# Performance work log

Hardware: AMD Instinct MI355X
Metric: run time of the kernel (lower is better)

The kernel has to match this reference:

```python
import jax, jax.numpy as jnp
import numpy as np

N, E, F_IN, F_OUT, K = 10000, 640000, 256, 64, 4


def setup_inputs() -> dict:
    key = jax.random.key(0)
    ks = jax.random.split(key, 8)
    feat = jax.random.normal(ks[0], (N, F_IN), dtype=jnp.float32)
    feat_a = jax.random.normal(ks[1], (N, F_IN), dtype=jnp.float32)
    edge_index = jax.random.randint(ks[2], (2, E), 0, N)
    graph_neigh = jax.random.uniform(ks[3], (N, N), dtype=jnp.float32)
    W = jax.random.normal(ks[4], ((K + 1) * F_IN, F_OUT), dtype=jnp.float32) * 0.05
    Wb = jax.random.normal(ks[5], (F_OUT, F_OUT), dtype=jnp.float32) * 0.05
    b = jnp.zeros((), dtype=jnp.float32)
    return {"feat": feat, "feat_a": feat_a, "edge_index": edge_index,
            "graph_neigh": graph_neigh, "W": W, "Wb": Wb, "b": b}


def _sym_norm(edge_index, num_nodes):
    # add_remaining_self_loops with all-ones weights: drop existing self-loops,
    # append a weight-1 self loop per node (fill_value=1, improved=False)
    row, col = edge_index[0], edge_index[1]
    w = jnp.where(row == col, 0.0, 1.0).astype(jnp.float32)
    loop = jnp.arange(num_nodes)
    row = jnp.concatenate([row, loop])
    col = jnp.concatenate([col, loop])
    w = jnp.concatenate([w, jnp.ones((num_nodes,), jnp.float32)])
    deg = jax.ops.segment_sum(w, row, num_segments=num_nodes)
    dis = jnp.where(deg > 0, jax.lax.rsqrt(deg), 0.0)  # inf -> 0
    norm = dis[row] * w * dis[col]
    return row, col, norm


def _comb_unweighted(x, row, col, norm, k_hops):
    # K-hop propagation: out[dst] += norm * x[src]; concat hops 0..K
    xs = [x]
    for _ in range(k_hops):
        msg = norm[:, None] * xs[-1][row]          # gather + scale  [E', F]
        xs.append(jax.ops.segment_sum(msg, col, num_segments=x.shape[0]))
    return jnp.concatenate(xs, axis=1)             # [N, F*(K+1)]


def _avg_readout(emb, mask):
    vsum = mask @ emb                              # [N, F_OUT]
    row_sum = jnp.sum(mask, axis=1, keepdims=True)
    g = vsum / row_sum
    nrm = jnp.linalg.norm(g, axis=1, keepdims=True)
    return g / jnp.maximum(nrm, 1e-12)             # F.normalize p=2


def _disc(c, h_pl, h_mi, Wb, b):
    # nn.Bilinear(n_h, n_h, 1): sc = h^T Wb c + b, per node
    sc1 = jnp.einsum('nd,de,ne->n', h_pl, Wb, c) + b
    sc2 = jnp.einsum('nd,de,ne->n', h_mi, Wb, c) + b
    return jnp.stack([sc1, sc2], axis=1)           # [N, 2]


def reference(feat, feat_a, edge_index, graph_neigh, W, Wb, b):
    row, col, norm = _sym_norm(edge_index, feat.shape[0])
    h = _comb_unweighted(feat, row, col, norm, K) @ W
    h_a = _comb_unweighted(feat_a, row, col, norm, K) @ W
    emb = jax.nn.relu(h)
    emb_a = jax.nn.relu(h_a)
    g = jax.nn.sigmoid(_avg_readout(emb, graph_neigh))
    g_a = jax.nn.sigmoid(_avg_readout(emb_a, graph_neigh))
    ret = _disc(g, emb, emb_a, Wb, b)
    ret_a = _disc(g_a, emb_a, emb, Wb, b)
    return emb, ret, ret_a
```

## Files before the change

kernel.cpp:

```cpp
#include <hip/hip_runtime.h>
#include <hip/hip_bf16.h>
#include <hip/hip_fp16.h>

typedef float f32x4 __attribute__((ext_vector_type(4)));
typedef short s16x8 __attribute__((ext_vector_type(8)));
typedef unsigned int u32x4 __attribute__((ext_vector_type(4)));

#define F_IN 256
#define F_OUT 64
#define KSPLIT 9
#define HBLK 120

static __device__ __forceinline__ short f2bf(float f){
  union { float f; unsigned u; } x; x.f = f;
  unsigned r = (x.u + 0x7FFFu + ((x.u >> 16) & 1u)) >> 16;
  return (short)r;
}

static __device__ __forceinline__ unsigned pack_rtne(float f0, float f1){
  return ((unsigned)(unsigned short)f2bf(f0)) | ((unsigned)(unsigned short)f2bf(f1) << 16);
}

static __device__ __forceinline__ unsigned pack_trunc(float f0, float f1){
  return (__float_as_uint(f0) >> 16) | (__float_as_uint(f1) & 0xFFFF0000u);
}

static __device__ __forceinline__ float bf_lo(unsigned u){ return __uint_as_float(u << 16); }
static __device__ __forceinline__ float bf_hi(unsigned u){ return __uint_as_float(u & 0xFFFF0000u); }
static __device__ __forceinline__ float h16(unsigned u){
  return __half2float(__ushort_as_half((unsigned short)(u >> 16)));
}

union FragU { u32x4 u; s16x8 s; };


__global__ void wt_kernel(const float* __restrict__ W, short* __restrict__ WT){
  int idx = blockIdx.x * blockDim.x + threadIdx.x;
  if (idx < 5 * 64 * 256){
    int k = idx & 255, c = (idx >> 8) & 63, by = idx >> 14;
    WT[idx] = f2bf(W[(size_t)(by * 256 + k) * 64 + c]);
  }
}


__global__ __launch_bounds__(1024) void hist_kernel(const int* __restrict__ ei, int E,
                                                    unsigned* __restrict__ blkcntP, int n){
  __shared__ unsigned bins[10240];
  int tid = threadIdx.x;
  int per = (E + HBLK - 1) / HBLK;
  int e0 = blockIdx.x * per, e1 = min(E, e0 + per);

  for (int i = tid; i < n; i += 1024) bins[i] = 0u;
  __syncthreads();
  for (int e = e0 + tid; e < e1; e += 1024){
    int r = ei[e], c = ei[E + e];
    if (r != c){
      atomicAdd(&bins[c], 1u);
      atomicAdd(&bins[r], 0x10000u);
    }
  }
  __syncthreads();
  for (int i = tid; i < n; i += 1024)
    blkcntP[(size_t)blockIdx.x * n + i] = bins[i];
}


__global__ void sumcnt_kernel(const unsigned* __restrict__ blkcntP,
                              int* __restrict__ counts, int* __restrict__ deg, int n){
  int bin = blockIdx.x * blockDim.x + threadIdx.x;
  if (bin >= n) return;
  int cc = 0, rc = 0;
  #pragma unroll 8
  for (int blk = 0; blk < HBLK; ++blk){
    unsigned v = blkcntP[(size_t)blk * n + bin];
    cc += (int)(v & 0xFFFFu);
    rc += (int)(v >> 16);
  }
  counts[bin] = cc;
  deg[bin] = rc;
}


__global__ __launch_bounds__(1024) void scan_kernel(const int* __restrict__ counts,
                                                    const int* __restrict__ deg,
                                                    float* __restrict__ dis,
                                                    float* __restrict__ selfnorm,
                                                    int* __restrict__ offsets, int n){
  const int C = 10;
  __shared__ int vals[10240];
  __shared__ int wsums[16];
  int tid = threadIdx.x, wid = tid >> 6, lane = tid & 63;
  for (int i = tid; i < 10240; i += 1024) vals[i] = (i < n) ? counts[i] : 0;
  for (int i = tid; i < n; i += 1024){
    float d = (float)(deg[i] + 1);
    dis[i] = rsqrtf(d);
    selfnorm[i] = 1.0f / d;
  }
  __syncthreads();
  int base = tid * C;
  int s = 0;
  #pragma unroll
  for (int i = 0; i < C; ++i) s += vals[base + i];
  int x = s;
  #pragma unroll
  for (int off = 1; off < 64; off <<= 1){
    int y = __shfl_up(x, off);
    if (lane >= off) x += y;
  }
  if (lane == 63) wsums[wid] = x;
  __syncthreads();
  if (wid == 0){
    int v = (lane < 16) ? wsums[lane] : 0;
    int xx = v;
    #pragma unroll
    for (int off = 1; off < 16; off <<= 1){
      int y = __shfl_up(xx, off);
      if (lane >= off) xx += y;
    }
    if (lane < 16) wsums[lane] = xx - v;
  }
  __syncthreads();
  int run = (x - s) + wsums[wid];
  if (tid == 1023) offsets[n] = run + s;
  #pragma unroll
  for (int i = 0; i < C; ++i){ int v = vals[base + i]; vals[base + i] = run; run += v; }
  __syncthreads();
  for (int i = tid; i < 10240; i += 1024)
    if (i < n) offsets[i] = vals[i];
}


__global__ void blkbase_kernel(const int* __restrict__ offsets, const unsigned* __restrict__ blkcntP,
                               int* __restrict__ blkbase, int n){
  int bin = blockIdx.x * blockDim.x + threadIdx.x;
  if (bin >= n) return;
  int run = offsets[bin];
  #pragma unroll 8
  for (int blk = 0; blk < HBLK; ++blk){
    blkbase[(size_t)blk * n + bin] = run;
    run += (int)(blkcntP[(size_t)blk * n + bin] & 0xFFFFu);
  }
}


__global__ __launch_bounds__(1024) void fill_kernel(const int* __restrict__ ei, int E,
                                                    const float* __restrict__ dis,
                                                    const int* __restrict__ blkbase,
                                                    unsigned* __restrict__ csr, int n){
  __shared__ int bins[10240];
  int tid = threadIdx.x;
  int per = (E + HBLK - 1) / HBLK;
  int e0 = blockIdx.x * per, e1 = min(E, e0 + per);
  for (int i = tid; i < n; i += 1024) bins[i] = blkbase[(size_t)blockIdx.x * n + i];
  __syncthreads();
  for (int e = e0 + tid; e < e1; e += 1024){
    int r = ei[e], c = ei[E + e];
    if (r == c) continue;
    int pos = atomicAdd(&bins[c], 1);
    unsigned h = (unsigned)__half_as_ushort(__float2half(dis[r] * dis[c]));
    csr[pos] = (unsigned)r | (h << 16);
  }
}


__global__ __launch_bounds__(320) void fgemm_kernel(const float* __restrict__ X0,
                                                    const float* __restrict__ X1,
                                                    const short* __restrict__ WT,
                                                    float* __restrict__ Yc0,
                                                    unsigned* __restrict__ YcB,
                                                    short* __restrict__ t0bf, int M){
  __shared__ float Xs[16][260];
  int tid = threadIdx.x;
  int w = tid >> 6, l = tid & 63, lr = l & 15, g = l >> 4;
  int row0 = blockIdx.x * 16, bz = blockIdx.y;
  const float* X = bz ? X1 : X0;
  for (int i = tid; i < 1024; i += 320){
    int r = i >> 6, c4 = (i & 63) << 2;
    *(f32x4*)&Xs[r][c4] = *(const f32x4*)(X + (size_t)(row0 + r) * F_IN + c4);
  }
  __syncthreads();

  s16x8 afr[8];
  #pragma unroll
  for (int it = 0; it < 8; ++it){
    f32x4 x0 = *(const f32x4*)&Xs[lr][it * 32 + g * 8];
    f32x4 x1 = *(const f32x4*)&Xs[lr][it * 32 + g * 8 + 4];
    FragU af;
    af.u[0] = pack_rtne(x0[0], x0[1]); af.u[1] = pack_rtne(x0[2], x0[3]);
    af.u[2] = pack_rtne(x1[0], x1[1]); af.u[3] = pack_rtne(x1[2], x1[3]);
    afr[it] = af.s;
  }

  int by = w;
  f32x4 acc[4];
  #pragma unroll
  for (int ct = 0; ct < 4; ++ct) acc[ct] = (f32x4){0,0,0,0};
  const s16x8* bp[4];
  #pragma unroll
  for (int ct = 0; ct < 4; ++ct)
    bp[ct] = (const s16x8*)(WT + ((size_t)by * 64 + ct * 16 + lr) * F_IN + g * 8);
  #pragma unroll
  for (int it = 0; it < 8; ++it)
    #pragma unroll
    for (int ct = 0; ct < 4; ++ct)
      acc[ct] = __builtin_amdgcn_mfma_f32_16x16x32_bf16(afr[it], bp[ct][it * 4], acc[ct], 0, 0, 0);

  if (by == 0){
    float* yp = Yc0 + (size_t)bz * 64;
    #pragma unroll
    for (int ct = 0; ct < 4; ++ct)
      #pragma unroll
      for (int i = 0; i < 4; ++i)
        yp[(size_t)(row0 + g * 4 + i) * 128 + ct * 16 + lr] = acc[ct][i];
  } else if (by <= 3){
    unsigned* yb = YcB + (size_t)(by - 1) * (M >> 1) * 128 + (size_t)bz * 64;
    #pragma unroll
    for (int ct = 0; ct < 4; ++ct)
      #pragma unroll
      for (int i = 0; i < 4; i += 2){
        int grow = row0 + g * 4 + i;
        yb[(size_t)(grow >> 1) * 128 + ct * 16 + lr] = pack_rtne(acc[ct][i], acc[ct][i + 1]);
      }
  } else {
    short* tb = t0bf + (size_t)bz * 64;
    #pragma unroll
    for (int ct = 0; ct < 4; ++ct)
      #pragma unroll
      for (int i = 0; i < 4; ++i)
        tb[(size_t)(row0 + g * 4 + i) * 128 + ct * 16 + lr] = f2bf(acc[ct][i]);
  }
}


__global__ __launch_bounds__(256) void gather_kernel(const void* __restrict__ Yk,
    const unsigned* __restrict__ tinb, const int* __restrict__ offsets,
    const unsigned* __restrict__ csr, const float* __restrict__ selfnorm,
    unsigned* __restrict__ toutb, float* __restrict__ toutf, int n, int wantf, int ykbf){
  int wid = threadIdx.x >> 6, lane = threadIdx.x & 63;
  int node = blockIdx.x * 4 + wid;
  if (node >= n) return;
  int e0 = offsets[node], e1 = offsets[node + 1];
  float sn = selfnorm[node];
  unsigned t0 = tinb[(size_t)node * 64 + lane];
  float ykx, yky;
  if (ykbf){
    const unsigned* yp = (const unsigned*)Yk + (size_t)(node >> 1) * 128 + lane * 2;
    unsigned u0 = yp[0], u1 = yp[1];
    if (node & 1){ ykx = bf_hi(u0); yky = bf_hi(u1); }
    else         { ykx = bf_lo(u0); yky = bf_lo(u1); }
  } else {
    float2 yk = ((const float2*)Yk)[(size_t)node * 64 + lane];
    ykx = yk.x; yky = yk.y;
  }
  float ax = ykx + sn * bf_lo(t0);
  float ay = yky + sn * bf_hi(t0);
  int i = e0;
  for (; i + 8 <= e1; i += 8){
    unsigned q0 = csr[i],   q1 = csr[i+1], q2 = csr[i+2], q3 = csr[i+3];
    unsigned q4 = csr[i+4], q5 = csr[i+5], q6 = csr[i+6], q7 = csr[i+7];
    unsigned v0 = tinb[(size_t)(q0 & 0xFFFFu) * 64 + lane];
    unsigned v1 = tinb[(size_t)(q1 & 0xFFFFu) * 64 + lane];
    unsigned v2 = tinb[(size_t)(q2 & 0xFFFFu) * 64 + lane];
    unsigned v3 = tinb[(size_t)(q3 & 0xFFFFu) * 64 + lane];
    unsigned v4 = tinb[(size_t)(q4 & 0xFFFFu) * 64 + lane];
    unsigned v5 = tinb[(size_t)(q5 & 0xFFFFu) * 64 + lane];
    unsigned v6 = tinb[(size_t)(q6 & 0xFFFFu) * 64 + lane];
    unsigned v7 = tinb[(size_t)(q7 & 0xFFFFu) * 64 + lane];
    float w0 = h16(q0), w1 = h16(q1), w2 = h16(q2), w3 = h16(q3);
    float w4 = h16(q4), w5 = h16(q5), w6 = h16(q6), w7 = h16(q7);
    ax += w0 * bf_lo(v0); ay += w0 * bf_hi(v0);
    ax += w1 * bf_lo(v1); ay += w1 * bf_hi(v1);
    ax += w2 * bf_lo(v2); ay += w2 * bf_hi(v2);
    ax += w3 * bf_lo(v3); ay += w3 * bf_hi(v3);
    ax += w4 * bf_lo(v4); ay += w4 * bf_hi(v4);
    ax += w5 * bf_lo(v5); ay += w5 * bf_hi(v5);
    ax += w6 * bf_lo(v6); ay += w6 * bf_hi(v6);
    ax += w7 * bf_lo(v7); ay += w7 * bf_hi(v7);
  }
  for (; i + 4 <= e1; i += 4){
    unsigned q0 = csr[i], q1 = csr[i+1], q2 = csr[i+2], q3 = csr[i+3];
    unsigned v0 = tinb[(size_t)(q0 & 0xFFFFu) * 64 + lane];
    unsigned v1 = tinb[(size_t)(q1 & 0xFFFFu) * 64 + lane];
    unsigned v2 = tinb[(size_t)(q2 & 0xFFFFu) * 64 + lane];
    unsigned v3 = tinb[(size_t)(q3 & 0xFFFFu) * 64 + lane];
    float w0 = h16(q0), w1 = h16(q1), w2 = h16(q2), w3 = h16(q3);
    ax += w0 * bf_lo(v0); ay += w0 * bf_hi(v0);
    ax += w1 * bf_lo(v1); ay += w1 * bf_hi(v1);
    ax += w2 * bf_lo(v2); ay += w2 * bf_hi(v2);
    ax += w3 * bf_lo(v3); ay += w3 * bf_hi(v3);
  }
  for (; i < e1; ++i){
    unsigned q = csr[i];
    float w = h16(q);
    unsigned v = tinb[(size_t)(q & 0xFFFFu) * 64 + lane];
    ax += w * bf_lo(v); ay += w * bf_hi(v);
  }
  if (wantf){
    float2 r; r.x = ax; r.y = ay;
    ((float2*)toutf)[(size_t)node * 64 + lane] = r;
  } else {
    toutb[(size_t)node * 64 + lane] = pack_rtne(ax, ay);
  }
}


__global__ __launch_bounds__(256) void relu_trans_kernel(const float* __restrict__ u,
    float* __restrict__ emb, float* __restrict__ emb_a, short* __restrict__ embBT, int n){
  __shared__ short lds[128 * 72];
  int t = threadIdx.x;
  int node0 = blockIdx.x * 64;
  int nl = t >> 2;
  int f0 = (t & 3) * 32;
  int node = node0 + nl;
  if (node < n){
    const f32x4* up = (const f32x4*)(u + (size_t)node * 128 + f0);
    float* dst = (f0 < 64) ? (emb + (size_t)node * 64 + f0)
                           : (emb_a + (size_t)node * 64 + (f0 - 64));
    #pragma unroll
    for (int j4 = 0; j4 < 8; ++j4){
      f32x4 v = up[j4];
      #pragma unroll
      for (int e = 0; e < 4; ++e){
        float x = v[e] > 0.0f ? v[e] : 0.0f;
        v[e] = x;
        lds[(f0 + j4 * 4 + e) * 72 + nl] = f2bf(x);
      }
      ((f32x4*)dst)[j4] = v;
    }
  }
  __syncthreads();
  int f = t >> 1, c0 = (t & 1) * 32;
  short* op = embBT + (size_t)f * n + node0 + c0;
  const short* lp = lds + f * 72 + c0;
  if (node0 + 64 <= n){
    #pragma unroll
    for (int j = 0; j < 4; ++j)
      *(s16x8*)(op + j * 8) = *(const s16x8*)(lp + j * 8);
  } else {
    for (int j = 0; j < 32; ++j)
      if (node0 + c0 + j < n) op[j] = lp[j];
  }
}


__global__ __launch_bounds__(256, 3) void readout_kernel(const float* __restrict__ mask,
    const short* __restrict__ embBT, unsigned* __restrict__ vsumP, int n){
  __shared__ float Ab[2][128][32];
  __shared__ short Bb[2][128][32];
  int t = threadIdx.x;
  int w = t >> 6, l = t & 63, lr = l & 15, g = l >> 4;
  int row0 = blockIdx.x * 128;
  int ks = blockIdx.y;

  int steps_total = (n + 31) >> 5;
  int per = steps_total / KSPLIT, rem = steps_total % KSPLIT;
  int sbeg = ks * per + (ks < rem ? ks : rem);
  int scnt = per + (ks < rem ? 1 : 0);
  bool tail = ((sbeg + scnt) == steps_total) && ((n & 31) != 0);
  int nf = scnt - (tail ? 1 : 0);
  int kb0 = sbeg << 5;

  int aswz = ((l & 7) ^ ((l >> 3) & 7)) << 2;
  const float* asrc[4];
  #pragma unroll
  for (int j = 0; j < 4; ++j){
    int ar = row0 + w * 32 + j * 8 + (l >> 3);
    asrc[j] = mask + (size_t)min(ar, n - 1) * n + aswz;
  }
  int bcol = w * 32 + (l >> 2);
  int bswz = ((l & 3) ^ ((l >> 3) & 3)) << 3;
  const short* bsrc0 = embBT + (size_t)bcol * n + bswz;
  const short* bsrc1 = embBT + (size_t)(bcol + 16) * n + bswz;

  #define GLDS(gp, lp) __builtin_amdgcn_global_load_lds( \
      (const __attribute__((address_space(1))) void*)(const void*)(gp), \
      (__attribute__((address_space(3))) void*)(void*)(lp), 16, 0, 0)
  #define STAGE(kb, bi) do{ \
    GLDS(asrc[0] + (kb), &Ab[bi][w * 32     ][0]); \
    GLDS(asrc[1] + (kb), &Ab[bi][w * 32 +  8][0]); \
    GLDS(asrc[2] + (kb), &Ab[bi][w * 32 + 16][0]); \
    GLDS(asrc[3] + (kb), &Ab[bi][w * 32 + 24][0]); \
    GLDS(bsrc0 + (kb), &Bb[bi][w * 32     ][0]); \
    GLDS(bsrc1 + (kb), &Bb[bi][w * 32 + 16][0]); \
  }while(0)

  f32x4 acc[2][8];
  #pragma unroll
  for (int rt = 0; rt < 2; ++rt)
    #pragma unroll
    for (int ct = 0; ct < 8; ++ct) acc[rt][ct] = (f32x4){0,0,0,0};

  if (nf > 0) STAGE(kb0, 0);
  if (nf > 1) STAGE(kb0 + 32, 1);

  for (int s = 0; s < nf; ++s){
    if (s + 1 < nf) asm volatile("s_waitcnt vmcnt(6)" ::: "memory");
    else            asm volatile("s_waitcnt vmcnt(0)" ::: "memory");
    __builtin_amdgcn_s_barrier();
    int cur = s & 1;
    s16x8 bfr[8];
    #pragma unroll
    for (int ct = 0; ct < 8; ++ct)
      bfr[ct] = *(const s16x8*)&Bb[cur][ct * 16 + lr][(g ^ ((lr >> 1) & 3)) << 3];
    #pragma unroll
    for (int rt = 0; rt < 2; ++rt){
      f32x4 x0 = *(const f32x4*)&Ab[cur][w * 32 + rt * 16 + lr][((2 * g)     ^ (lr & 7)) << 2];
      f32x4 x1 = *(const f32x4*)&Ab[cur][w * 32 + rt * 16 + lr][((2 * g + 1) ^ (lr & 7)) << 2];
      FragU af;
      af.u[0] = pack_trunc(x0[0], x0[1]); af.u[1] = pack_trunc(x0[2], x0[3]);
      af.u[2] = pack_trunc(x1[0], x1[1]); af.u[3] = pack_trunc(x1[2], x1[3]);
      #pragma unroll
      for (int ct = 0; ct < 8; ++ct)
        acc[rt][ct] = __builtin_amdgcn_mfma_f32_16x16x32_bf16(af.s, bfr[ct], acc[rt][ct], 0, 0, 0);
    }
    asm volatile("s_waitcnt lgkmcnt(0)" ::: "memory");
    __builtin_amdgcn_s_barrier();
    if (s + 2 < nf) STAGE(kb0 + (s + 2) * 32, cur);
  }
  #undef STAGE
  #undef GLDS

  if (tail){
    int kb = kb0 + nf * 32;
    int kleft = n - kb;
    const s16x8 bz = {0,0,0,0,0,0,0,0};
    s16x8 bfr[8];
    #pragma unroll
    for (int ct = 0; ct < 8; ++ct)
      bfr[ct] = (g * 8 < kleft) ? *(const s16x8*)(embBT + (size_t)(ct * 16 + lr) * n + kb + g * 8) : bz;
    #pragma unroll
    for (int rt = 0; rt < 2; ++rt){
      FragU af; af.u = (u32x4){0,0,0,0};
      int r = row0 + w * 32 + rt * 16 + lr;
      if (g * 8 < kleft && r < n){
        const f32x4* p = (const f32x4*)(mask + (size_t)r * n + kb + g * 8);
        f32x4 r0 = p[0], r1 = p[1];
        af.u[0] = pack_trunc(r0[0], r0[1]); af.u[1] = pack_trunc(r0[2], r0[3]);
        af.u[2] = pack_trunc(r1[0], r1[1]); af.u[3] = pack_trunc(r1[2], r1[3]);
      }
      #pragma unroll
      for (int ct = 0; ct < 8; ++ct)
        acc[rt][ct] = __builtin_amdgcn_mfma_f32_16x16x32_bf16(af.s, bfr[ct], acc[rt][ct], 0, 0, 0);
    }
  }

  unsigned* vs = vsumP + (size_t)ks * (n >> 1) * 128;
  #pragma unroll
  for (int rt = 0; rt < 2; ++rt){
    int rbase = row0 + w * 32 + rt * 16;
    #pragma unroll
    for (int ct = 0; ct < 8; ++ct)
      #pragma unroll
      for (int i = 0; i < 4; i += 2){
        int gr = rbase + g * 4 + i;
        if (gr < n)
          vs[(size_t)(gr >> 1) * 128 + ct * 16 + lr] = pack_rtne(acc[rt][ct][i], acc[rt][ct][i + 1]);
      }
  }
}


__global__ __launch_bounds__(256) void gnorm_disc_kernel(const unsigned* __restrict__ vsumP,
    const float* __restrict__ emb, const float* __restrict__ emb_a,
    const float* __restrict__ Wb, const float* __restrict__ bptr,
    float* __restrict__ ret, float* __restrict__ reta, int n){
  __shared__ float Wl[64][65];
  int t = threadIdx.x;
  for (int i = t; i < 4096; i += 256) Wl[i >> 6][i & 63] = Wb[i];
  __syncthreads();
  int wid = t >> 6, lane = t & 63;
  int node = blockIdx.x * 4 + wid;
  if (node >= n) return;

  size_t stride = (size_t)(n >> 1) * 128;
  size_t rowoff = (size_t)(node >> 1) * 128;
  bool hi = (node & 1) != 0;
  float v1 = 0.0f, v2 = 0.0f;
  #pragma unroll
  for (int ks = 0; ks < KSPLIT; ++ks){
    unsigned a = vsumP[ks * stride + rowoff + lane];
    unsigned b = vsumP[ks * stride + rowoff + 64 + lane];
    v1 += hi ? bf_hi(a) : bf_lo(a);
    v2 += hi ? bf_hi(b) : bf_lo(b);
  }
  float s1 = v1 * v1, s2 = v2 * v2;
  for (int off = 32; off >= 1; off >>= 1){
    s1 += __shfl_xor(s1, off);
    s2 += __shfl_xor(s2, off);
  }
  float i1 = v1 / fmaxf(sqrtf(s1), 1e-12f);
  float i2 = v2 / fmaxf(sqrtf(s2), 1e-12f);
  float g1 = 1.0f / (1.0f + expf(-i1));
  float g2 = 1.0f / (1.0f + expf(-i2));

  float e1 = emb[(size_t)node * 64 + lane];
  float e2 = emb_a[(size_t)node * 64 + lane];
  float u1 = 0.0f, u2 = 0.0f;
  for (int e = 0; e < 64; ++e){
    float wv = Wl[lane][e];
    u1 += wv * __shfl(g1, e);
    u2 += wv * __shfl(g2, e);
  }
  float p1 = e1 * u1, p2 = e2 * u1, p3 = e2 * u2, p4 = e1 * u2;
  for (int off = 32; off >= 1; off >>= 1){
    p1 += __shfl_xor(p1, off); p2 += __shfl_xor(p2, off);
    p3 += __shfl_xor(p3, off); p4 += __shfl_xor(p4, off);
  }
  if (lane == 0){
    float b = bptr[0];
    ret[(size_t)node * 2 + 0]  = p1 + b;
    ret[(size_t)node * 2 + 1]  = p2 + b;
    reta[(size_t)node * 2 + 0] = p3 + b;
    reta[(size_t)node * 2 + 1] = p4 + b;
  }
}


extern "C" void kernel_launch(void* const* d_in, const int* in_sizes, int n_in,
                              void* d_out, int out_size, void* d_ws, size_t ws_size,
                              hipStream_t stream) {
  const float* feat   = (const float*)d_in[0];
  const float* feat_a = (const float*)d_in[1];
  const int*   ei     = (const int*)d_in[2];
  const float* mask   = (const float*)d_in[3];
  const float* W      = (const float*)d_in[4];
  const float* Wb     = (const float*)d_in[5];
  const float* bsc    = (const float*)d_in[6];
  const int n = in_sizes[0] / F_IN;
  const int E = in_sizes[2] / 2;
  const size_t sl128 = (size_t)n * 128;

  float* out  = (float*)d_out;
  float* ret  = out + (size_t)n * F_OUT;
  float* reta = ret + (size_t)n * 2;

  char* wsb = (char*)d_ws;
  size_t off = 0;
  #define WSALLOC(ptr, T, cnt) T* ptr = (T*)(wsb + off); off = (off + sizeof(T)*(size_t)(cnt) + 255) & ~(size_t)255
  WSALLOC(deg, int, n);
  WSALLOC(counts, int, n);
  WSALLOC(offs, int, n + 1);
  WSALLOC(dis, float, n);
  WSALLOC(selfnorm, float, n);
  WSALLOC(csr, unsigned, E);
  WSALLOC(blkcntP, unsigned, (size_t)HBLK * n);
  WSALLOC(blkbase, int, (size_t)HBLK * n);
  WSALLOC(WT, short, 5 * 64 * 256);
  WSALLOC(Yc0, float, sl128);
  WSALLOC(YcB, unsigned, (size_t)3 * (n >> 1) * 128);
  WSALLOC(t0bf, short, sl128);
  WSALLOC(tb0, unsigned, (size_t)n * 64);
  WSALLOC(tb1, unsigned, (size_t)n * 64);
  WSALLOC(u1, float, sl128);
  WSALLOC(emb_a, float, (size_t)n * F_OUT);
  WSALLOC(embBT, short, (size_t)128 * n);
  WSALLOC(vsumP, unsigned, (size_t)KSPLIT * (n >> 1) * 128);
  (void)ws_size; (void)n_in; (void)out_size;

  wt_kernel<<<(5 * 64 * 256 + 255) / 256, 256, 0, stream>>>(W, WT);
  hist_kernel<<<HBLK, 1024, 0, stream>>>(ei, E, blkcntP, n);
  sumcnt_kernel<<<(n + 255) / 256, 256, 0, stream>>>(blkcntP, counts, deg, n);
  scan_kernel<<<1, 1024, 0, stream>>>(counts, deg, dis, selfnorm, offs, n);
  blkbase_kernel<<<(n + 255) / 256, 256, 0, stream>>>(offs, blkcntP, blkbase, n);
  fill_kernel<<<HBLK, 1024, 0, stream>>>(ei, E, dis, blkbase, csr, n);

  fgemm_kernel<<<dim3(n / 16, 2), 320, 0, stream>>>(feat, feat_a, WT, Yc0, YcB, t0bf, n);

  int gb = (n + 3) / 4;
  const size_t ybs = (size_t)(n >> 1) * 128;
  gather_kernel<<<gb, 256, 0, stream>>>(YcB + 2 * ybs, (unsigned*)t0bf, offs, csr, selfnorm, tb0, (float*)0, n, 0, 1);
  gather_kernel<<<gb, 256, 0, stream>>>(YcB + 1 * ybs, tb0, offs, csr, selfnorm, tb1, (float*)0, n, 0, 1);
  gather_kernel<<<gb, 256, 0, stream>>>(YcB + 0 * ybs, tb1, offs, csr, selfnorm, tb0, (float*)0, n, 0, 1);
  gather_kernel<<<gb, 256, 0, stream>>>(Yc0, tb0, offs, csr, selfnorm, (unsigned*)0, u1, n, 1, 0);
  relu_trans_kernel<<<(n + 63) / 64, 256, 0, stream>>>(u1, out, emb_a, embBT, n);

  readout_kernel<<<dim3((n + 127) / 128, KSPLIT), 256, 0, stream>>>(mask, embBT, vsumP, n);
  gnorm_disc_kernel<<<gb, 256, 0, stream>>>(vsumP, out, emb_a, Wb, bsc, ret, reta, n);
}
```

Baseline: 295.8 us.

## Restructure readout GEMM into single-wave blocks with triple-buffered barrier-free pipeline

The readout kernel changes from 256-thread blocks covering 128 mask rows to 64-thread, single-wave blocks covering 32 rows. Its LDS staging goes from double to triple buffering, and with one wave per block the workgroup barriers are dropped. The split-K factor rises from 9 to 13 to keep enough blocks in flight. The aim is to hide more of the streaming latency of the large fp32 mask read and remove barrier stalls. In exchange, each wave now loads the whole 128-column embedding tile itself, which is four times the B-operand traffic, and more partial sums are written for the reduction.

```diff
diff --git a/kernel.cpp b/kernel.cpp
--- a/kernel.cpp
+++ b/kernel.cpp
@@ -8,7 +8,7 @@
 
 #define F_IN 256
 #define F_OUT 64
-#define KSPLIT 9
+#define KSPLIT 13
 #define HBLK 120
 
 static __device__ __forceinline__ short f2bf(float f){
@@ -343,13 +343,12 @@
 }
 
 
-__global__ __launch_bounds__(256, 3) void readout_kernel(const float* __restrict__ mask,
+__global__ __launch_bounds__(64) void readout_kernel(const float* __restrict__ mask,
     const short* __restrict__ embBT, unsigned* __restrict__ vsumP, int n){
-  __shared__ float Ab[2][128][32];
-  __shared__ short Bb[2][128][32];
-  int t = threadIdx.x;
-  int w = t >> 6, l = t & 63, lr = l & 15, g = l >> 4;
-  int row0 = blockIdx.x * 128;
+  __shared__ float Ab[3][32][32];
+  __shared__ short Bb[3][128][32];
+  int l = threadIdx.x, lr = l & 15, g = l >> 4;
+  int row0 = blockIdx.x * 32;
   int ks = blockIdx.y;
 
   int steps_total = (n + 31) >> 5;
@@ -364,24 +363,31 @@
   const float* asrc[4];
   #pragma unroll
   for (int j = 0; j < 4; ++j){
-    int ar = row0 + w * 32 + j * 8 + (l >> 3);
+    int ar = row0 + j * 8 + (l >> 3);
     asrc[j] = mask + (size_t)min(ar, n - 1) * n + aswz;
   }
-  int bcol = w * 32 + (l >> 2);
   int bswz = ((l & 3) ^ ((l >> 3) & 3)) << 3;
-  const short* bsrc0 = embBT + (size_t)bcol * n + bswz;
-  const short* bsrc1 = embBT + (size_t)(bcol + 16) * n + bswz;
+  const short* bsrc[8];
+  #pragma unroll
+  for (int j = 0; j < 8; ++j)
+    bsrc[j] = embBT + (size_t)(j * 16 + (l >> 2)) * n + bswz;
 
   #define GLDS(gp, lp) __builtin_amdgcn_global_load_lds( \
       (const __attribute__((address_space(1))) void*)(const void*)(gp), \
       (__attribute__((address_space(3))) void*)(void*)(lp), 16, 0, 0)
   #define STAGE(kb, bi) do{ \
-    GLDS(asrc[0] + (kb), &Ab[bi][w * 32     ][0]); \
-    GLDS(asrc[1] + (kb), &Ab[bi][w * 32 +  8][0]); \
-    GLDS(asrc[2] + (kb), &Ab[bi][w * 32 + 16][0]); \
-    GLDS(asrc[3] + (kb), &Ab[bi][w * 32 + 24][0]); \
-    GLDS(bsrc0 + (kb), &Bb[bi][w * 32     ][0]); \
-    GLDS(bsrc1 + (kb), &Bb[bi][w * 32 + 16][0]); \
+    GLDS(asrc[0] + (kb), &Ab[bi][ 0][0]); \
+    GLDS(asrc[1] + (kb), &Ab[bi][ 8][0]); \
+    GLDS(asrc[2] + (kb), &Ab[bi][16][0]); \
+    GLDS(asrc[3] + (kb), &Ab[bi][24][0]); \
+    GLDS(bsrc[0] + (kb), &Bb[bi][  0][0]); \
+    GLDS(bsrc[1] + (kb), &Bb[bi][ 16][0]); \
+    GLDS(bsrc[2] + (kb), &Bb[bi][ 32][0]); \
+    GLDS(bsrc[3] + (kb), &Bb[bi][ 48][0]); \
+    GLDS(bsrc[4] + (kb), &Bb[bi][ 64][0]); \
+    GLDS(bsrc[5] + (kb), &Bb[bi][ 80][0]); \
+    GLDS(bsrc[6] + (kb), &Bb[bi][ 96][0]); \
+    GLDS(bsrc[7] + (kb), &Bb[bi][112][0]); \
   }while(0)
 
   f32x4 acc[2][8];
@@ -392,20 +398,21 @@
 
   if (nf > 0) STAGE(kb0, 0);
   if (nf > 1) STAGE(kb0 + 32, 1);
-
+  if (nf > 2) STAGE(kb0 + 64, 2);
+
+  int cur = 0;
   for (int s = 0; s < nf; ++s){
-    if (s + 1 < nf) asm volatile("s_waitcnt vmcnt(6)" ::: "memory");
-    else            asm volatile("s_waitcnt vmcnt(0)" ::: "memory");
-    __builtin_amdgcn_s_barrier();
-    int cur = s & 1;
+    if (s + 3 <= nf)      asm volatile("s_waitcnt vmcnt(24)" ::: "memory");
+    else if (s + 2 == nf) asm volatile("s_waitcnt vmcnt(12)" ::: "memory");
+    else                  asm volatile("s_waitcnt vmcnt(0)" ::: "memory");
     s16x8 bfr[8];
     #pragma unroll
     for (int ct = 0; ct < 8; ++ct)
       bfr[ct] = *(const s16x8*)&Bb[cur][ct * 16 + lr][(g ^ ((lr >> 1) & 3)) << 3];
     #pragma unroll
     for (int rt = 0; rt < 2; ++rt){
-      f32x4 x0 = *(const f32x4*)&Ab[cur][w * 32 + rt * 16 + lr][((2 * g)     ^ (lr & 7)) << 2];
-      f32x4 x1 = *(const f32x4*)&Ab[cur][w * 32 + rt * 16 + lr][((2 * g + 1) ^ (lr & 7)) << 2];
+      f32x4 x0 = *(const f32x4*)&Ab[cur][rt * 16 + lr][((2 * g)     ^ (lr & 7)) << 2];
+      f32x4 x1 = *(const f32x4*)&Ab[cur][rt * 16 + lr][((2 * g + 1) ^ (lr & 7)) << 2];
       FragU af;
       af.u[0] = pack_trunc(x0[0], x0[1]); af.u[1] = pack_trunc(x0[2], x0[3]);
       af.u[2] = pack_trunc(x1[0], x1[1]); af.u[3] = pack_trunc(x1[2], x1[3]);
@@ -414,8 +421,8 @@
         acc[rt][ct] = __builtin_amdgcn_mfma_f32_16x16x32_bf16(af.s, bfr[ct], acc[rt][ct], 0, 0, 0);
     }
     asm volatile("s_waitcnt lgkmcnt(0)" ::: "memory");
-    __builtin_amdgcn_s_barrier();
-    if (s + 2 < nf) STAGE(kb0 + (s + 2) * 32, cur);
+    if (s + 3 < nf) STAGE(kb0 + (s + 3) * 32, cur);
+    cur = (cur == 2) ? 0 : cur + 1;
   }
   #undef STAGE
   #undef GLDS
@@ -431,7 +438,7 @@
     #pragma unroll
     for (int rt = 0; rt < 2; ++rt){
       FragU af; af.u = (u32x4){0,0,0,0};
-      int r = row0 + w * 32 + rt * 16 + lr;
+      int r = row0 + rt * 16 + lr;
       if (g * 8 < kleft && r < n){
         const f32x4* p = (const f32x4*)(mask + (size_t)r * n + kb + g * 8);
         f32x4 r0 = p[0], r1 = p[1];
@@ -447,7 +454,7 @@
   unsigned* vs = vsumP + (size_t)ks * (n >> 1) * 128;
   #pragma unroll
   for (int rt = 0; rt < 2; ++rt){
-    int rbase = row0 + w * 32 + rt * 16;
+    int rbase = row0 + rt * 16;
     #pragma unroll
     for (int ct = 0; ct < 8; ++ct)
       #pragma unroll
@@ -574,6 +581,6 @@
   gather_kernel<<<gb, 256, 0, stream>>>(Yc0, tb0, offs, csr, selfnorm, (unsigned*)0, u1, n, 1, 0);
   relu_trans_kernel<<<(n + 63) / 64, 256, 0, stream>>>(u1, out, emb_a, embBT, n);
 
-  readout_kernel<<<dim3((n + 127) / 128, KSPLIT), 256, 0, stream>>>(mask, embBT, vsumP, n);
+  readout_kernel<<<dim3((n + 31) / 32, KSPLIT), 64, 0, stream>>>(mask, embBT, vsumP, n);
   gnorm_disc_kernel<<<gb, 256, 0, stream>>>(vsumP, out, emb_a, Wb, bsc, ret, reta, n);
 }
```

Measured after the change: 363.3 us. +22.8%, slower.
